# Performance work log

Measured on AMD Instinct MI355X. Metric: run time of the kernel, lower is better.

## Reference

```python
import jax, jax.numpy as jnp
import numpy as np

B, C_IN, T, DIM_H, HEADS, K = 64, 64, 512, 64, 2, 9
N = B * T            # graph nodes = batch * cycle_size
E = 524288           # edges (avg degree 16)
D = HEADS * DIM_H    # 128, GATv2 concat output
EPS = 1e-5
SLOPE = 0.2          # GATv2 leaky_relu negative slope


def setup_inputs() -> dict:
    key = jax.random.key(0)
    ks = jax.random.split(key, 12)
    s = 0.05
    return {
        'x': jax.random.normal(ks[0], (B, C_IN, T), jnp.float32),
        'edge_index': jax.random.randint(ks[1], (2, E), 0, N, jnp.int32),
        'bn0_g': jnp.ones((C_IN,), jnp.float32),
        'bn0_b': jnp.zeros((C_IN,), jnp.float32),
        'W_l': jax.random.normal(ks[2], (C_IN, D), jnp.float32) * s,
        'W_r': jax.random.normal(ks[3], (C_IN, D), jnp.float32) * s,
        'att': jax.random.normal(ks[4], (HEADS, DIM_H), jnp.float32) * s,
        'gat_b': jnp.zeros((D,), jnp.float32),
        'bn1_g': jnp.ones((D,), jnp.float32),
        'bn1_b': jnp.zeros((D,), jnp.float32),
        'conv_w': jax.random.normal(ks[5], (T, T, K), jnp.float32) * s,
        'conv_b': jnp.zeros((T,), jnp.float32),
        'bn2_g': jnp.ones((T,), jnp.float32),
        'bn2_b': jnp.zeros((T,), jnp.float32),
    }


def _bn(x, g, b, axes, shape):
    # BatchNorm1d in training mode: biased batch stats per channel
    m = jnp.mean(x, axes, keepdims=True)
    v = jnp.var(x, axes, keepdims=True)
    return (x - m) * jax.lax.rsqrt(v + EPS) * g.reshape(shape) + b.reshape(shape)


def _gatv2(x, edge_index, W_l, W_r, att, bias):
    # PyG GATv2Conv: out_i = sum_j softmax_j(att . leaky_relu(xl_j + xr_i)) * xl_j
    xl = (x @ W_l).reshape(N, HEADS, DIM_H)
    xr = (x @ W_r).reshape(N, HEADS, DIM_H)
    loops = jnp.arange(N, dtype=edge_index.dtype)  # add_self_loops=True
    src = jnp.concatenate([edge_index[0], loops])
    dst = jnp.concatenate([edge_index[1], loops])
    h = xl[src] + xr[dst]                       # [E+N, H, dh]
    h = jnp.where(h > 0, h, SLOPE * h)
    logits = jnp.einsum('ehd,hd->eh', h, att)   # [E+N, H]
    mmax = jax.ops.segment_max(logits, dst, num_segments=N)
    a = jnp.exp(logits - mmax[dst])
    z = jax.ops.segment_sum(a, dst, num_segments=N)
    alpha = a / z[dst]                          # scatter-softmax over incoming edges
    out = jax.ops.segment_sum(alpha[:, :, None] * xl[src], dst, num_segments=N)
    return out.reshape(N, D) + bias


def reference(x, edge_index, bn0_g, bn0_b, W_l, W_r, att, gat_b,
              bn1_g, bn1_b, conv_w, conv_b, bn2_g, bn2_b):
    # b0 (batch_size > 1), x: [B, C_IN, T]
    x = _bn(x, bn0_g, bn0_b, (0, 2), (1, C_IN, 1))
    # (skip_connection branch is dead code: its result is overwritten)
    # torch .view on contiguous [B,C,T] -> [B*T, C] == raw reshape
    xn = x.reshape(N, C_IN)
    xn = jax.nn.relu(_bn(_gatv2(xn, edge_index, W_l, W_r, att, gat_b),
                         bn1_g, bn1_b, (0,), (1, D)))
    x3 = xn.reshape(B, D, T)
    residual = x3
    xt = jnp.transpose(x3, (0, 2, 1))           # [B, T, D]: channels=T, length=D
    y = jax.lax.conv_general_dilated(xt, conv_w, (1,), 'SAME',
                                     dimension_numbers=('NCH', 'OIH', 'NCH'))
    y = y + conv_b[None, :, None]
    y = jax.nn.relu(_bn(y, bn2_g, bn2_b, (0, 2), (1, T, 1)))
    y = jnp.transpose(y, (0, 2, 1))             # [B, D, T]
    # dropout(p=0.1) is identity in eval
    return residual + y
```

## Files before the change

kernel.cpp:

```cpp
#include <hip/hip_runtime.h>
#include <stdint.h>

typedef __attribute__((ext_vector_type(8))) __bf16 bf16x8;
typedef __attribute__((ext_vector_type(4))) float f32x4;

#define DEVI __device__ __forceinline__

constexpr int Bn = 64, CIN = 64, Tn = 512, Nn = 32768, Dn = 128;
constexpr int En = 524288, ENn = En + Nn;
constexpr float EPSf = 1e-5f;

constexpr size_t OFF_XL   = 0;
constexpr size_t OFF_XR   = 8388608;
constexpr size_t OFF_GPAD = 16777216;
constexpr size_t OFF_WRE  = 25690112;
constexpr size_t OFF_WT   = 30408704;
constexpr size_t OFF_CNT  = 30441472;
constexpr size_t OFF_STAT = 34635776;
constexpr size_t OFF_SUM0 = OFF_STAT;
constexpr size_t OFF_SQ0  = OFF_STAT + 256;
constexpr size_t OFF_SUM1 = OFF_STAT + 512;
constexpr size_t OFF_SQ1  = OFF_STAT + 4608;
constexpr size_t OFF_SC2  = OFF_STAT + 8704;
constexpr size_t OFF_SH2  = OFF_STAT + 10752;
constexpr size_t OFF_BUCK = OFF_STAT + 12800;
constexpr size_t WS_NEED  = OFF_BUCK + 8388608;

DEVI float bf2f(unsigned short u){
  union { unsigned int u; float f; } x; x.u = ((unsigned int)u) << 16; return x.f;
}
DEVI unsigned short f2bf(float f){
  union { float f; unsigned int u; } x; x.f = f;
  unsigned int lsb = (x.u >> 16) & 1u;
  return (unsigned short)((x.u + 0x7fffu + lsb) >> 16);
}
DEVI void gl_lds16(const void* g, void* l){
  __builtin_amdgcn_global_load_lds(
      (const __attribute__((address_space(1))) unsigned int*)g,
      (__attribute__((address_space(3))) unsigned int*)l, 16, 0, 0);
}
DEVI float red32(float p){
  p += __shfl_xor(p, 1);  p += __shfl_xor(p, 2);  p += __shfl_xor(p, 4);
  p += __shfl_xor(p, 8);  p += __shfl_xor(p, 16);
  return p;
}
DEVI size_t gpad_addr(int b, int m, int d){
  int ig = m >> 2;
  int chunk = ((m & 3) << 1) | (d >> 6);
  int est = ((d & 63) + ((ig & 7) << 3)) & 63;
  return (size_t)b * 69632 + 2048 + (size_t)ig * 512 + (chunk << 6) + est;
}

__global__ void k_mark(float* out, int n){
  int i = blockIdx.x * 256 + threadIdx.x;
  if (i < n) out[i] = 1.0f;
}


__global__ void __launch_bounds__(256) k_stats(
    const float* __restrict__ x,
    float* __restrict__ sum0, float* __restrict__ sq0){
  __shared__ float l1[256], l2[256];
  int bl = blockIdx.x, t = threadIdx.x;
  int c = bl >> 2, q = bl & 3;
  const float4* x4 = (const float4*)x;
  float s = 0.f, ss = 0.f;
  #pragma unroll
  for (int j = 0; j < 8; ++j){
    int idx = t + j * 256;
    int b = (q << 4) + (idx >> 7);
    int tt4 = idx & 127;
    float4 v = x4[(size_t)b * 8192 + c * 128 + tt4];
    s  += (v.x + v.y) + (v.z + v.w);
    ss += (v.x * v.x + v.y * v.y) + (v.z * v.z + v.w * v.w);
  }
  l1[t] = s; l2[t] = ss; __syncthreads();
  for (int o = 128; o > 0; o >>= 1){
    if (t < o){ l1[t] += l1[t + o]; l2[t] += l2[t + o]; }
    __syncthreads();
  }
  if (t == 0){
    atomicAdd(sum0 + c, l1[0]);
    atomicAdd(sq0 + c, l2[0]);
  }
}

__global__ void __launch_bounds__(256) k_repack(
    const float* __restrict__ w, const float* __restrict__ wl,
    const float* __restrict__ wr,
    unsigned short* __restrict__ wre, unsigned short* __restrict__ wt){
  int b2 = blockIdx.x, t = threadIdx.x;
  if (b2 < 512){
    int to = b2;
    size_t rest_to = ((size_t)((to >> 7) * 2 + ((to >> 6) & 1)) << 12)
                   + ((size_t)((to >> 4) & 3) << 9)
                   + ((size_t)(to & 15) << 3);
    for (int it2 = 0; it2 < 2; ++it2){
      int ti = it2 * 256 + t;
      const float* src = w + ((size_t)to * 512 + ti) * 9;
      size_t idx = rest_to
                 + ((size_t)((ti >> 5) & 1) << 11)
                 + ((size_t)((ti >> 3) & 3) << 7)
                 + (size_t)(ti & 7);
      int c = ti >> 6;
      #pragma unroll
      for (int k = 0; k < 9; ++k)
        wre[idx + ((size_t)(k * 8 + c) << 15)] = f2bf(src[k]);
    }
  } else {
    int q = b2 - 512;
    int n = q * 64 + (t >> 2);
    int k0 = (t & 3) * 16;
    for (int k = k0; k < k0 + 16; ++k){
      float v = (n < 128) ? wl[k * 128 + n] : wr[k * 128 + (n - 128)];
      wt[n * 64 + k] = f2bf(v);
    }
  }
}

__global__ void __launch_bounds__(256) k_scatter(
    const int* __restrict__ ei,
    int* __restrict__ cnt, unsigned short* __restrict__ buck){
  int blk = blockIdx.x, t = threadIdx.x;
  int e0 = blk * 512 + t * 2;
  int2 sp = *(const int2*)(ei + e0);
  int2 dp = *(const int2*)(ei + En + e0);
  int slot0 = atomicAdd(cnt + (dp.x << 5), 1);
  int slot1 = atomicAdd(cnt + (dp.y << 5), 1);
  if (slot0 < 64) buck[(size_t)dp.x * 64 + slot0] = (unsigned short)sp.x;
  if (slot1 < 64) buck[(size_t)dp.y * 64 + slot1] = (unsigned short)sp.y;
}

__global__ void __launch_bounds__(256) k_xlxr(
    const float* __restrict__ x, const unsigned short* __restrict__ wt,
    const float* __restrict__ sum0, const float* __restrict__ sq0,
    const float* __restrict__ g0, const float* __restrict__ b0v,
    unsigned short* __restrict__ xl, unsigned short* __restrict__ xr){
  __shared__ unsigned short lA[128 * 64];
  __shared__ unsigned short lB[128 * 64];
  int bl = blockIdx.x, t = threadIdx.x;
  int m0 = (bl & 255) * 128;
  int nt = bl >> 8;
  {
    const unsigned short* gb = wt + nt * 128 * 64;
    #pragma unroll
    for (int i = 0; i < 4; ++i){
      int idx = t + i * 256;
      gl_lds16(gb + idx * 8, &lB[idx * 8]);
    }
  }
  {
    const float4* gx = (const float4*)(x + (size_t)m0 * 64);
    #pragma unroll
    for (int i = 0; i < 8; ++i){
      int idx = t + i * 256;
      float4 v = gx[idx];
      int row = idx >> 4;
      int ch = ((m0 + row) >> 3) & 63;
      float mean = sum0[ch] * (1.f / 32768.f);
      float var  = sq0[ch] * (1.f / 32768.f) - mean * mean;
      float sc = rsqrtf(var + EPSf) * g0[ch];
      float sh = b0v[ch] - mean * sc;
      unsigned int p0 = (unsigned int)f2bf(v.x * sc + sh) | ((unsigned int)f2bf(v.y * sc + sh) << 16);
      unsigned int p1 = (unsigned int)f2bf(v.z * sc + sh) | ((unsigned int)f2bf(v.w * sc + sh) << 16);
      *(uint2*)&lA[idx * 4] = make_uint2(p0, p1);
    }
  }
  __syncthreads();
  int w = t >> 6, lane = t & 63;
  int wm = (w & 1) * 64, wn = (w >> 1) * 64;
  int lrow = lane & 15, quad = lane >> 4;
  const f32x4 fz = {0.f, 0.f, 0.f, 0.f};
  f32x4 acc[4][4];
  #pragma unroll
  for (int i = 0; i < 4; ++i)
    #pragma unroll
    for (int j = 0; j < 4; ++j) acc[i][j] = fz;
  #pragma unroll
  for (int kk = 0; kk < 2; ++kk){
    bf16x8 a[4], bfr[4];
    #pragma unroll
    for (int i = 0; i < 4; ++i){
      a[i]   = *(const bf16x8*)&lA[(wm + i * 16 + lrow) * 64 + kk * 32 + quad * 8];
      bfr[i] = *(const bf16x8*)&lB[(wn + i * 16 + lrow) * 64 + kk * 32 + quad * 8];
    }
    #pragma unroll
    for (int i = 0; i < 4; ++i)
      #pragma unroll
      for (int j = 0; j < 4; ++j)
        acc[i][j] = __builtin_amdgcn_mfma_f32_16x16x32_bf16(a[i], bfr[j], acc[i][j], 0, 0, 0);
  }
  unsigned short* outb = nt ? xr : xl;
  #pragma unroll
  for (int i = 0; i < 4; ++i)
    #pragma unroll
    for (int j = 0; j < 4; ++j)
      #pragma unroll
      for (int r = 0; r < 4; ++r){
        int row = m0 + wm + i * 16 + quad * 4 + r;
        int col = wn + j * 16 + lrow;
        outb[row * 128 + col] = f2bf(acc[i][j][r]);
      }
}

__global__ void __launch_bounds__(256) k_gat(
    const unsigned short* __restrict__ xl, const unsigned short* __restrict__ xr,
    const float* __restrict__ att,
    const int* __restrict__ cnt, const unsigned short* __restrict__ buck,
    unsigned short* __restrict__ gpad,
    float* __restrict__ sum1, float* __restrict__ sq1){
  __shared__ float S[4][128], Q[4][128];
  int t = threadIdx.x;
  int wv = t >> 6, lane = t & 63;
  int dst = blockIdx.x * 4 + wv;
  float2 pa = *(const float2*)(att + (lane << 1));
  float a0 = pa.x, a1 = pa.y;
  unsigned int pr = *(const unsigned int*)(xr + (size_t)dst * 128 + (lane << 1));
  float r0 = bf2f((unsigned short)(pr & 0xffffu)), r1 = bf2f((unsigned short)(pr >> 16));
  const unsigned short* bk = buck + (size_t)dst * 64;
  int deg = cnt[dst << 5]; deg = deg > 64 ? 64 : deg;
  float z = 0.f, ac0 = 0.f, ac1 = 0.f;
  int i = 0;
  for (; i + 4 <= deg; i += 4){
    int s0 = bk[i], s1 = bk[i + 1], s2 = bk[i + 2], s3 = bk[i + 3];
    unsigned int px0 = *(const unsigned int*)(xl + (size_t)s0 * 128 + (lane << 1));
    unsigned int px1 = *(const unsigned int*)(xl + (size_t)s1 * 128 + (lane << 1));
    unsigned int px2 = *(const unsigned int*)(xl + (size_t)s2 * 128 + (lane << 1));
    unsigned int px3 = *(const unsigned int*)(xl + (size_t)s3 * 128 + (lane << 1));
    float x00 = bf2f((unsigned short)(px0 & 0xffffu)), x01 = bf2f((unsigned short)(px0 >> 16));
    float x10 = bf2f((unsigned short)(px1 & 0xffffu)), x11 = bf2f((unsigned short)(px1 >> 16));
    float x20 = bf2f((unsigned short)(px2 & 0xffffu)), x21 = bf2f((unsigned short)(px2 >> 16));
    float x30 = bf2f((unsigned short)(px3 & 0xffffu)), x31 = bf2f((unsigned short)(px3 >> 16));
    float h, p0, p1, p2, p3;
    h = x00 + r0; h = fmaxf(h, 0.2f * h); p0 = h * a0;
    h = x01 + r1; h = fmaxf(h, 0.2f * h); p0 += h * a1;
    h = x10 + r0; h = fmaxf(h, 0.2f * h); p1 = h * a0;
    h = x11 + r1; h = fmaxf(h, 0.2f * h); p1 += h * a1;
    h = x20 + r0; h = fmaxf(h, 0.2f * h); p2 = h * a0;
    h = x21 + r1; h = fmaxf(h, 0.2f * h); p2 += h * a1;
    h = x30 + r0; h = fmaxf(h, 0.2f * h); p3 = h * a0;
    h = x31 + r1; h = fmaxf(h, 0.2f * h); p3 += h * a1;
    p0 += __shfl_xor(p0, 1);  p1 += __shfl_xor(p1, 1);
    p2 += __shfl_xor(p2, 1);  p3 += __shfl_xor(p3, 1);
    p0 += __shfl_xor(p0, 2);  p1 += __shfl_xor(p1, 2);
    p2 += __shfl_xor(p2, 2);  p3 += __shfl_xor(p3, 2);
    p0 += __shfl_xor(p0, 4);  p1 += __shfl_xor(p1, 4);
    p2 += __shfl_xor(p2, 4);  p3 += __shfl_xor(p3, 4);
    p0 += __shfl_xor(p0, 8);  p1 += __shfl_xor(p1, 8);
    p2 += __shfl_xor(p2, 8);  p3 += __shfl_xor(p3, 8);
    p0 += __shfl_xor(p0, 16); p1 += __shfl_xor(p1, 16);
    p2 += __shfl_xor(p2, 16); p3 += __shfl_xor(p3, 16);
    float w0 = __expf(p0), w1 = __expf(p1), w2 = __expf(p2), w3 = __expf(p3);
    z += (w0 + w1) + (w2 + w3);
    ac0 += w0 * x00; ac0 += w1 * x10; ac0 += w2 * x20; ac0 += w3 * x30;
    ac1 += w0 * x01; ac1 += w1 * x11; ac1 += w2 * x21; ac1 += w3 * x31;
  }
  for (; i < deg + 1; ++i){
    int s = (i < deg) ? (int)bk[i] : dst;
    unsigned int px = *(const unsigned int*)(xl + (size_t)s * 128 + (lane << 1));
    float x0 = bf2f((unsigned short)(px & 0xffffu)), x1 = bf2f((unsigned short)(px >> 16));
    float h0 = x0 + r0; h0 = fmaxf(h0, 0.2f * h0);
    float h1 = x1 + r1; h1 = fmaxf(h1, 0.2f * h1);
    float p = red32(h0 * a0 + h1 * a1);
    float w = __expf(p);
    z += w; ac0 += w * x0; ac1 += w * x1;
  }
  float inv = (z > 0.f) ? 1.f / z : 0.f;
  float o0 = ac0 * inv, o1 = ac1 * inv;
  size_t off = gpad_addr(dst >> 9, dst & 511, lane << 1);
  *(unsigned int*)(gpad + off) =
      (unsigned int)f2bf(o0) | ((unsigned int)f2bf(o1) << 16);
  S[wv][lane * 2] = o0; S[wv][lane * 2 + 1] = o1;
  Q[wv][lane * 2] = o0 * o0; Q[wv][lane * 2 + 1] = o1 * o1;
  __syncthreads();
  int rep = (blockIdx.x & 7) << 7;
  if (t < 128){
    atomicAdd(sum1 + rep + t, (S[0][t] + S[1][t]) + (S[2][t] + S[3][t]));
  } else {
    int c = t - 128;
    atomicAdd(sq1 + rep + c, (Q[0][c] + Q[1][c]) + (Q[2][c] + Q[3][c]));
  }
}

__global__ void __launch_bounds__(256) k_bn1_apply(
    unsigned short* __restrict__ gpad,
    const float* __restrict__ sums, const float* __restrict__ sumsq,
    const float* __restrict__ g, const float* __restrict__ bb){
  int bl = blockIdx.x, t = threadIdx.x;
  if (bl >= 4096){
    int idx = (bl - 4096) * 256 + t;
    int b = idx >> 10, r = idx & 1023;
    int region = r >> 9, rp = r & 511;
    size_t off = (size_t)b * 69632 + (region ? 67584 : 0) + rp * 4;
    *(uint2*)(gpad + off) = make_uint2(0u, 0u);
    return;
  }
  int gi = bl * 256 + t;
  int f0 = gi * 4;
  int b = f0 >> 16, q = f0 & 65535;
  int m = q >> 7, d0 = q & 127;
  float sc[4], sh[4];
  #pragma unroll
  for (int j = 0; j < 4; ++j){
    int d = d0 + j;
    float s = 0.f, ssq = 0.f;
    #pragma unroll
    for (int r = 0; r < 8; ++r){
      s   += sums[(r << 7) + d];
      ssq += sumsq[(r << 7) + d];
    }
    float mean = s / 32768.f;
    float var  = ssq / 32768.f - mean * mean;
    float rs = rsqrtf(var + EPSf) * g[d];
    sc[j] = rs; sh[j] = bb[d] - mean * rs;
  }
  unsigned short* gp = gpad + gpad_addr(b, m, d0);
  uint2 v = *(const uint2*)gp;
  float o0 = fmaxf(0.f, bf2f((unsigned short)(v.x & 0xffffu)) * sc[0] + sh[0]);
  float o1 = fmaxf(0.f, bf2f((unsigned short)(v.x >> 16))     * sc[1] + sh[1]);
  float o2 = fmaxf(0.f, bf2f((unsigned short)(v.y & 0xffffu)) * sc[2] + sh[2]);
  float o3 = fmaxf(0.f, bf2f((unsigned short)(v.y >> 16))     * sc[3] + sh[3]);
  unsigned int p0 = (unsigned int)f2bf(o0) | ((unsigned int)f2bf(o1) << 16);
  unsigned int p1 = (unsigned int)f2bf(o2) | ((unsigned int)f2bf(o3) << 16);
  *(uint2*)gp = make_uint2(p0, p1);
}

__global__ void __launch_bounds__(256) k_conv(
    const unsigned short* __restrict__ wre,
    const unsigned short* __restrict__ gpad,
    unsigned short* __restrict__ y0, unsigned short* __restrict__ y1){
  __shared__ unsigned short lB[3][128 * 64];
  int t = threadIdx.x;
  int id  = blockIdx.x;
  int xcd = id & 7, u = id >> 3;
  int z    = xcd & 1;
  int b    = (xcd >> 1) * 16 + (u >> 2);
  int tile = u & 3;
  int to0  = tile * 128;
  int w = t >> 6, lane = t & 63;
  int wm = (w & 1) * 64, wn = (w >> 1) * 64;
  int mh = w & 1;
  int lrow = lane & 15, quad = lane >> 4;
  const f32x4 fz = {0.f, 0.f, 0.f, 0.f};
  f32x4 acc[4][4];
  #pragma unroll
  for (int i = 0; i < 4; ++i)
    #pragma unroll
    for (int j = 0; j < 4; ++j) acc[i][j] = fz;
  const unsigned short* gbb = gpad + (size_t)b * 69632;
  int og[4], ol[4];
  #pragma unroll
  for (int i = 0; i < 4; ++i){
    int idx = t + i * 256;
    og[i] = (idx >> 3) * 512 + (idx & 7) * 8;
    ol[i] = idx * 8;
  }
  int s0 = z * 36;
  const unsigned short* wlane = wre + ((size_t)((tile << 1) | mh) << 12) + (lane << 3);

  bf16x8 aA[8], aB[8];
  {
    int k0 = s0 >> 3, c0 = s0 & 7;
    const unsigned short* gB = gbb + k0 * 512 + c0 * 64;
    #pragma unroll
    for (int i = 0; i < 4; ++i) gl_lds16(gB + og[i], &lB[0][ol[i]]);
  }
  __builtin_amdgcn_sched_barrier(0);
  #pragma unroll
  for (int f = 0; f < 8; ++f)
    aA[f] = *(const bf16x8*)(wlane + ((size_t)s0 << 15) + (f << 9));
  __builtin_amdgcn_sched_barrier(0);
  {
    int s1 = s0 + 1;
    int k1 = s1 >> 3, c1 = s1 & 7;
    const unsigned short* gB = gbb + k1 * 512 + c1 * 64;
    #pragma unroll
    for (int i = 0; i < 4; ++i) gl_lds16(gB + og[i], &lB[1][ol[i]]);
  }
  __builtin_amdgcn_sched_barrier(0);
  #pragma unroll
  for (int f = 0; f < 8; ++f)
    aB[f] = *(const bf16x8*)(wlane + ((size_t)(s0 + 1) << 15) + (f << 9));
  __builtin_amdgcn_sched_barrier(0);

#define STEP(IT, RD, WR, A_) do {                                          \
    int it_ = (IT);                                                        \
    int s_  = s0 + it_;                                                    \
    if (it_ < 35) { asm volatile("s_waitcnt vmcnt(12)" ::: "memory"); }    \
    else          { asm volatile("s_waitcnt vmcnt(0)" ::: "memory"); }     \
    __builtin_amdgcn_sched_barrier(0);                                     \
    __builtin_amdgcn_s_barrier();                                          \
    __builtin_amdgcn_sched_barrier(0);                                     \
    if (it_ < 34){                                                         \
      int sn_ = s_ + 2;                                                    \
      int kn_ = sn_ >> 3, cn_ = sn_ & 7;                                   \
      const unsigned short* gB_ = gbb + kn_ * 512 + cn_ * 64;              \
      _Pragma("unroll")                                                    \
      for (int i = 0; i < 4; ++i) gl_lds16(gB_ + og[i], &lB[WR][ol[i]]);   \
    }                                                                      \
    __builtin_amdgcn_sched_barrier(0);                                     \
    {                                                                      \
      int k_ = s_ >> 3;                                                    \
      int rb_ = (k_ + 4 + lrow) & 7;                                       \
      const unsigned short* lb_ = lB[RD];                                  \
      _Pragma("unroll")                                                    \
      for (int kk = 0; kk < 2; ++kk){                                      \
        int colB = ((kk << 5) + (quad << 3) + (rb_ << 3)) & 63;            \
        bf16x8 bfr[4];                                                     \
        _Pragma("unroll")                                                  \
        for (int j = 0; j < 4; ++j)                                        \
          bfr[j] = *(const bf16x8*)&lb_[(wn + j * 16 + lrow) * 64 + colB]; \
        _Pragma("unroll")                                                  \
        for (int i = 0; i < 4; ++i)                                        \
          _Pragma("unroll")                                                \
          for (int j = 0; j < 4; ++j)                                      \
            acc[i][j] = __builtin_amdgcn_mfma_f32_16x16x32_bf16(           \
                A_[kk * 4 + i], bfr[j], acc[i][j], 0, 0, 0);               \
      }                                                                    \
    }                                                                      \
    __builtin_amdgcn_sched_barrier(0);                                     \
    if (it_ < 34){                                                         \
      _Pragma("unroll")                                                    \
      for (int f = 0; f < 8; ++f)                                          \
        A_[f] = *(const bf16x8*)(wlane + ((size_t)(s_ + 2) << 15) + (f << 9)); \
    }                                                                      \
    __builtin_amdgcn_sched_barrier(0);                                     \
  } while (0)

  for (int g = 0; g < 6; ++g){
    STEP(g * 6 + 0, 0, 2, aA);
    STEP(g * 6 + 1, 1, 0, aB);
    STEP(g * 6 + 2, 2, 1, aA);
    STEP(g * 6 + 3, 0, 2, aB);
    STEP(g * 6 + 4, 1, 0, aA);
    STEP(g * 6 + 5, 2, 1, aB);
  }
#undef STEP

  unsigned short* yo = z ? y1 : y0;
  #pragma unroll
  for (int i = 0; i < 4; ++i)
    #pragma unroll
    for (int j = 0; j < 4; ++j)
      #pragma unroll
      for (int r = 0; r < 4; ++r){
        int to = to0 + wm + i * 16 + quad * 4 + r;
        int p  = wn + j * 16 + lrow;
        yo[((size_t)b * 512 + to) * 128 + p] = f2bf(acc[i][j][r]);
      }
}

__global__ void k_bn2_stats(const unsigned short* __restrict__ y0,
                            const unsigned short* __restrict__ y1,
                            const float* __restrict__ g, const float* __restrict__ bb,
                            float* __restrict__ scale, float* __restrict__ shift){
  int to = blockIdx.x, t = threadIdx.x;
  int p = t & 127, b0 = t >> 7;
  float s = 0.f, ss = 0.f;
  for (int b = b0; b < 64; b += 2){
    size_t idx = ((size_t)b * 512 + to) * 128 + p;
    float v = bf2f(y0[idx]) + bf2f(y1[idx]);
    s += v; ss += v * v;
  }
  __shared__ float l1[256], l2[256];
  l1[t] = s; l2[t] = ss; __syncthreads();
  for (int o = 128; o > 0; o >>= 1){
    if (t < o){ l1[t] += l1[t + o]; l2[t] += l2[t + o]; }
    __syncthreads();
  }
  if (t == 0){
    float mean = l1[0] / 8192.f;
    float var  = l2[0] / 8192.f - mean * mean;
    float rs = rsqrtf(var + EPSf) * g[to];
    scale[to] = rs;
    shift[to] = bb[to] - mean * rs;
  }
}

__global__ void __launch_bounds__(256) k_final(
    const unsigned short* __restrict__ y0, const unsigned short* __restrict__ y1,
    const unsigned short* __restrict__ gpad,
    const float* __restrict__ scale, const float* __restrict__ shift,
    float* __restrict__ out){
  __shared__ float lt[32][33];
  int jt = blockIdx.x, it = blockIdx.y, b = blockIdx.z;
  int j0 = jt * 32, i0 = it * 32;
  int t = threadIdx.x;
  #pragma unroll
  for (int q = 0; q < 4; ++q){
    int li = t + q * 256;
    int r = li >> 5, cc = li & 31;
    int j = j0 + r;
    size_t idx = ((size_t)b * 512 + j) * 128 + i0 + cc;
    float v = bf2f(y0[idx]) + bf2f(y1[idx]);
    lt[r][cc] = fmaxf(0.f, v * scale[j] + shift[j]);
  }
  __syncthreads();
  const unsigned short* gbb = gpad + (size_t)b * 69632 + 2048;
  #pragma unroll
  for (int q = 0; q < 4; ++q){
    int li = t + q * 256;
    int ii = li >> 5, jj = li & 31;
    int i = i0 + ii, j = j0 + jj;
    int est = ((j & 63) + ((i & 7) << 3)) & 63;
    float res = bf2f(gbb[(size_t)i * 512 + ((j >> 6) << 6) + est]);
    size_t o = (size_t)b * 65536 + (size_t)i * 512 + j;
    out[o] = res + lt[jj][ii];
  }
}

extern "C" void kernel_launch(void* const* d_in, const int* in_sizes, int n_in,
                              void* d_out, int out_size, void* d_ws, size_t ws_size,
                              hipStream_t stream){
  const float* x     = (const float*)d_in[0];
  const int*   ei    = (const int*)d_in[1];
  const float* bn0g  = (const float*)d_in[2];
  const float* bn0b  = (const float*)d_in[3];
  const float* Wl    = (const float*)d_in[4];
  const float* Wr    = (const float*)d_in[5];
  const float* att   = (const float*)d_in[6];
  const float* bn1g  = (const float*)d_in[8];
  const float* bn1b  = (const float*)d_in[9];
  const float* convw = (const float*)d_in[10];
  const float* bn2g  = (const float*)d_in[12];
  const float* bn2b  = (const float*)d_in[13];
  float* out = (float*)d_out;

  if (ws_size < WS_NEED){
    k_mark<<<(out_size + 255) / 256, 256, 0, stream>>>(out, out_size);
    return;
  }
  char* ws = (char*)d_ws;
  unsigned short* xl   = (unsigned short*)(ws + OFF_XL);
  unsigned short* xr   = (unsigned short*)(ws + OFF_XR);
  unsigned short* y0   = (unsigned short*)(ws + OFF_XL);
  unsigned short* y1   = (unsigned short*)(ws + OFF_XR);
  unsigned short* gpad = (unsigned short*)(ws + OFF_GPAD);
  unsigned short* wre  = (unsigned short*)(ws + OFF_WRE);
  unsigned short* wt   = (unsigned short*)(ws + OFF_WT);
  int*            cnt  = (int*)(ws + OFF_CNT);
  unsigned short* buck = (unsigned short*)(ws + OFF_BUCK);
  float*          sum0 = (float*)(ws + OFF_SUM0);
  float*          sq0  = (float*)(ws + OFF_SQ0);
  float*          sum1 = (float*)(ws + OFF_SUM1);
  float*          sq1  = (float*)(ws + OFF_SQ1);
  float*          sc2  = (float*)(ws + OFF_SC2);
  float*          sh2  = (float*)(ws + OFF_SH2);

  hipMemsetAsync(cnt, 0, 4203008, stream);

  k_scatter<<<1024, 256, 0, stream>>>(ei, cnt, buck);
  k_stats<<<256, 256, 0, stream>>>(x, sum0, sq0);
  k_repack<<<516, 256, 0, stream>>>(convw, Wl, Wr, wre, wt);
  k_xlxr<<<512, 256, 0, stream>>>(x, wt, sum0, sq0, bn0g, bn0b, xl, xr);
  k_gat<<<8192, 256, 0, stream>>>(xl, xr, att, cnt, buck, gpad, sum1, sq1);
  k_bn1_apply<<<4352, 256, 0, stream>>>(gpad, sum1, sq1, bn1g, bn1b);
  k_conv<<<512, 256, 0, stream>>>(wre, gpad, y0, y1);
  k_bn2_stats<<<512, 256, 0, stream>>>(y0, y1, bn2g, bn2b, sc2, sh2);
  k_final<<<dim3(16, 4, 64), 256, 0, stream>>>(y0, y1, gpad, sc2, sh2, out);

  (void)in_sizes; (void)n_in;
}
```

Before: 251.9 us.

## Halve conv output tile and use double buffering to raise occupancy

Each conv block now computes a 64-row output tile instead of 128, so the grid doubles to 1024 blocks and the accumulator and A-fragment registers are halved. The B-operand LDS ring drops from triple to double buffering, the prefetch distance shrinks from two steps to one with a full vmcnt(0) wait each step, and launch bounds request 4 blocks per CU. The aim is more resident waves and more parallelism to hide latency. The cost is that each B tile is loaded from global twice as often and the pipeline is shallower, which exposes more load latency per step.

Result: slower. 260.0 us (+3.2%).

```diff
diff --git a/kernel.cpp b/kernel.cpp
--- a/kernel.cpp
+++ b/kernel.cpp
@@ -55,7 +55,6 @@
   int i = blockIdx.x * 256 + threadIdx.x;
   if (i < n) out[i] = 1.0f;
 }
-
 
 __global__ void __launch_bounds__(256) k_stats(
     const float* __restrict__ x,
@@ -325,26 +324,26 @@
   *(uint2*)gp = make_uint2(p0, p1);
 }
 
-__global__ void __launch_bounds__(256) k_conv(
+__global__ void __launch_bounds__(256, 4) k_conv(
     const unsigned short* __restrict__ wre,
     const unsigned short* __restrict__ gpad,
     unsigned short* __restrict__ y0, unsigned short* __restrict__ y1){
-  __shared__ unsigned short lB[3][128 * 64];
+  __shared__ unsigned short lB[2][128 * 64];
   int t = threadIdx.x;
   int id  = blockIdx.x;
   int xcd = id & 7, u = id >> 3;
-  int z    = xcd & 1;
-  int b    = (xcd >> 1) * 16 + (u >> 2);
-  int tile = u & 3;
-  int to0  = tile * 128;
+  int z     = xcd & 1;
+  int b     = (xcd >> 1) * 16 + (u >> 3);
+  int tile8 = u & 7;
+  int to0   = tile8 * 64;
   int w = t >> 6, lane = t & 63;
-  int wm = (w & 1) * 64, wn = (w >> 1) * 64;
-  int mh = w & 1;
+  int sub = w & 1;
+  int wn  = (w >> 1) * 64;
   int lrow = lane & 15, quad = lane >> 4;
   const f32x4 fz = {0.f, 0.f, 0.f, 0.f};
-  f32x4 acc[4][4];
-  #pragma unroll
-  for (int i = 0; i < 4; ++i)
+  f32x4 acc[2][4];
+  #pragma unroll
+  for (int i = 0; i < 2; ++i)
     #pragma unroll
     for (int j = 0; j < 4; ++j) acc[i][j] = fz;
   const unsigned short* gbb = gpad + (size_t)b * 69632;
@@ -356,9 +355,13 @@
     ol[i] = idx * 8;
   }
   int s0 = z * 36;
-  const unsigned short* wlane = wre + ((size_t)((tile << 1) | mh) << 12) + (lane << 3);
-
-  bf16x8 aA[8], aB[8];
+  const unsigned short* wlane = wre + ((size_t)tile8 << 12) + (lane << 3);
+  int fo[4];
+  #pragma unroll
+  for (int q = 0; q < 4; ++q)
+    fo[q] = ((q >> 1) * 4 + sub * 2 + (q & 1)) << 9;
+
+  bf16x8 aA[4], aB[4];
   {
     int k0 = s0 >> 3, c0 = s0 & 7;
     const unsigned short* gB = gbb + k0 * 512 + c0 * 64;
@@ -367,42 +370,33 @@
   }
   __builtin_amdgcn_sched_barrier(0);
   #pragma unroll
-  for (int f = 0; f < 8; ++f)
-    aA[f] = *(const bf16x8*)(wlane + ((size_t)s0 << 15) + (f << 9));
+  for (int q = 0; q < 4; ++q)
+    aA[q] = *(const bf16x8*)(wlane + ((size_t)s0 << 15) + fo[q]);
   __builtin_amdgcn_sched_barrier(0);
-  {
-    int s1 = s0 + 1;
-    int k1 = s1 >> 3, c1 = s1 & 7;
-    const unsigned short* gB = gbb + k1 * 512 + c1 * 64;
-    #pragma unroll
-    for (int i = 0; i < 4; ++i) gl_lds16(gB + og[i], &lB[1][ol[i]]);
-  }
-  __builtin_amdgcn_sched_barrier(0);
-  #pragma unroll
-  for (int f = 0; f < 8; ++f)
-    aB[f] = *(const bf16x8*)(wlane + ((size_t)(s0 + 1) << 15) + (f << 9));
-  __builtin_amdgcn_sched_barrier(0);
-
-#define STEP(IT, RD, WR, A_) do {                                          \
+
+#define STEP(IT, AC, AN) do {                                              \
     int it_ = (IT);                                                        \
     int s_  = s0 + it_;                                                    \
-    if (it_ < 35) { asm volatile("s_waitcnt vmcnt(12)" ::: "memory"); }    \
-    else          { asm volatile("s_waitcnt vmcnt(0)" ::: "memory"); }     \
+    asm volatile("s_waitcnt vmcnt(0)" ::: "memory");                       \
     __builtin_amdgcn_sched_barrier(0);                                     \
     __builtin_amdgcn_s_barrier();                                          \
     __builtin_amdgcn_sched_barrier(0);                                     \
-    if (it_ < 34){                                                         \
-      int sn_ = s_ + 2;                                                    \
+    if (it_ < 35){                                                         \
+      int sn_ = s_ + 1;                                                    \
       int kn_ = sn_ >> 3, cn_ = sn_ & 7;                                   \
       const unsigned short* gB_ = gbb + kn_ * 512 + cn_ * 64;              \
       _Pragma("unroll")                                                    \
-      for (int i = 0; i < 4; ++i) gl_lds16(gB_ + og[i], &lB[WR][ol[i]]);   \
+      for (int i = 0; i < 4; ++i)                                          \
+        gl_lds16(gB_ + og[i], &lB[(it_ + 1) & 1][ol[i]]);                  \
+      _Pragma("unroll")                                                    \
+      for (int q = 0; q < 4; ++q)                                          \
+        AN[q] = *(const bf16x8*)(wlane + ((size_t)sn_ << 15) + fo[q]);     \
     }                                                                      \
     __builtin_amdgcn_sched_barrier(0);                                     \
     {                                                                      \
       int k_ = s_ >> 3;                                                    \
       int rb_ = (k_ + 4 + lrow) & 7;                                       \
-      const unsigned short* lb_ = lB[RD];                                  \
+      const unsigned short* lb_ = lB[it_ & 1];                             \
       _Pragma("unroll")                                                    \
       for (int kk = 0; kk < 2; ++kk){                                      \
         int colB = ((kk << 5) + (quad << 3) + (rb_ << 3)) & 63;            \
@@ -411,40 +405,30 @@
         for (int j = 0; j < 4; ++j)                                        \
           bfr[j] = *(const bf16x8*)&lb_[(wn + j * 16 + lrow) * 64 + colB]; \
         _Pragma("unroll")                                                  \
-        for (int i = 0; i < 4; ++i)                                        \
+        for (int i = 0; i < 2; ++i)                                        \
           _Pragma("unroll")                                                \
           for (int j = 0; j < 4; ++j)                                      \
             acc[i][j] = __builtin_amdgcn_mfma_f32_16x16x32_bf16(           \
-                A_[kk * 4 + i], bfr[j], acc[i][j], 0, 0, 0);               \
+                AC[kk * 2 + i], bfr[j], acc[i][j], 0, 0, 0);               \
       }                                                                    \
     }                                                                      \
     __builtin_amdgcn_sched_barrier(0);                                     \
-    if (it_ < 34){                                                         \
-      _Pragma("unroll")                                                    \
-      for (int f = 0; f < 8; ++f)                                          \
-        A_[f] = *(const bf16x8*)(wlane + ((size_t)(s_ + 2) << 15) + (f << 9)); \
-    }                                                                      \
-    __builtin_amdgcn_sched_barrier(0);                                     \
   } while (0)
 
-  for (int g = 0; g < 6; ++g){
-    STEP(g * 6 + 0, 0, 2, aA);
-    STEP(g * 6 + 1, 1, 0, aB);
-    STEP(g * 6 + 2, 2, 1, aA);
-    STEP(g * 6 + 3, 0, 2, aB);
-    STEP(g * 6 + 4, 1, 0, aA);
-    STEP(g * 6 + 5, 2, 1, aB);
+  for (int g = 0; g < 18; ++g){
+    STEP(2 * g,     aA, aB);
+    STEP(2 * g + 1, aB, aA);
   }
 #undef STEP
 
   unsigned short* yo = z ? y1 : y0;
   #pragma unroll
-  for (int i = 0; i < 4; ++i)
+  for (int i = 0; i < 2; ++i)
     #pragma unroll
     for (int j = 0; j < 4; ++j)
       #pragma unroll
       for (int r = 0; r < 4; ++r){
-        int to = to0 + wm + i * 16 + quad * 4 + r;
+        int to = to0 + sub * 32 + i * 16 + quad * 4 + r;
         int p  = wn + j * 16 + lrow;
         yo[((size_t)b * 512 + to) * 128 + p] = f2bf(acc[i][j][r]);
       }
@@ -555,7 +539,7 @@
   k_xlxr<<<512, 256, 0, stream>>>(x, wt, sum0, sq0, bn0g, bn0b, xl, xr);
   k_gat<<<8192, 256, 0, stream>>>(xl, xr, att, cnt, buck, gpad, sum1, sq1);
   k_bn1_apply<<<4352, 256, 0, stream>>>(gpad, sum1, sq1, bn1g, bn1b);
-  k_conv<<<512, 256, 0, stream>>>(wre, gpad, y0, y1);
+  k_conv<<<1024, 256, 0, stream>>>(wre, gpad, y0, y1);
   k_bn2_stats<<<512, 256, 0, stream>>>(y0, y1, bn2g, bn2b, sc2, sh2);
   k_final<<<dim3(16, 4, 64), 256, 0, stream>>>(y0, y1, gpad, sc2, sh2, out);
 
```
